# Performance work log

Measured on AMD Instinct MI355X. Metric: run time of the kernel, lower is better.

## Reference

```python
import jax, jax.numpy as jnp
import numpy as np


def _adder2d(x, w, stride, padding):
    """AdderNet 'convolution': out[b,o,i,j] = -sum_p |patch[b,p,i,j] - w[o,p]|.

    x: [B, C, H, W], w: [O, C, kh, kw]. Patches are extracted in (C, kh, kw)
    channel-major order, matching torch.nn.functional.unfold / w.reshape(O, -1).
    """
    O, C, kh, kw = w.shape
    patches = jax.lax.conv_general_dilated_patches(
        x, (kh, kw), (stride, stride), [(padding, padding), (padding, padding)])
    B, P, Ho, Wo = patches.shape  # P = C*kh*kw
    p = patches.reshape(B, P, Ho * Wo)
    wf = w.reshape(O, P)

    def per_out(wo):  # sequential over small O to avoid a [B,O,P,L] blowup
        return -jnp.sum(jnp.abs(p - wo[None, :, None]), axis=1)  # [B, L]

    out = jax.lax.map(per_out, wf)  # [O, B, L]
    return jnp.transpose(out, (1, 0, 2)).reshape(B, O, Ho, Wo)


def setup_inputs() -> dict:
    key = jax.random.key(0)
    ks = jax.random.split(key, 5)
    x = jax.random.normal(ks[0], (4096, 1, 28, 28), dtype=jnp.float32)
    w1 = jax.random.normal(ks[1], (16, 1, 3, 3), dtype=jnp.float32)
    w2 = jax.random.normal(ks[2], (32, 16, 3, 3), dtype=jnp.float32)
    w3 = jax.random.normal(ks[3], (16, 32, 3, 3), dtype=jnp.float32)
    w4 = jax.random.normal(ks[4], (10, 16, 3, 3), dtype=jnp.float32)
    return {"x": x, "w1": w1, "w2": w2, "w3": w3, "w4": w4}


def reference(x, w1, w2, w3, w4):
    h = x - 0.5
    h = jax.nn.relu((_adder2d(h, w1, 2, 0) + 10.0) / 4.0)   # [B,16,13,13]
    h = jax.nn.relu((_adder2d(h, w2, 2, 1) + 130.0) / 8.0)  # [B,32,7,7]
    h = jax.nn.relu((_adder2d(h, w3, 2, 1) + 280.0) / 16.0)  # [B,16,4,4]
    h = _adder2d(h, w4, 2, 0)                                # [B,10,1,1]
    h = h.reshape(h.shape[0], -1)                            # [B,10]
    return jax.nn.log_softmax(h, axis=1)
```

## Files before the change

### kernel.cpp

```cpp
#include <hip/hip_runtime.h>
#include <math.h>


#if defined(__has_builtin)
#if __has_builtin(__builtin_amdgcn_sad_u16)
#define HAS_SAD 1
#endif
#endif

__device__ __forceinline__ unsigned sadu16(unsigned a, unsigned b, unsigned acc) {
#ifdef HAS_SAD
  return __builtin_amdgcn_sad_u16(a, b, acc);
#else
  int al = (int)(a & 0xFFFFu), ah = (int)(a >> 16);
  int bl = (int)(b & 0xFFFFu), bh = (int)(b >> 16);
  return acc + (unsigned)(al > bl ? al - bl : bl - al)
             + (unsigned)(ah > bh ? ah - bh : bh - ah);
#endif
}

__device__ __forceinline__ unsigned quant(float v) {
  return (unsigned)fmaf(v, 1024.0f, 8192.5f);
}

#define QPAD 0x20002000u

__global__ void adder_prep(const float* __restrict__ w1, const float* __restrict__ w2,
                           const float* __restrict__ w3, const float* __restrict__ w4,
                           unsigned* __restrict__ qw) {
  int k = blockIdx.x * 256 + threadIdx.x;
  if (k < 96) {
    int o = k / 6, r = k % 6, kh = r >> 1, h = r & 1;
    const float* p = w1 + o * 9 + kh * 3;
    qw[k] = h ? quant(p[2]) : (quant(p[0]) | (quant(p[1]) << 16));
  } else if (k < 2400) {
    int k2 = k - 96, m = k2 / 288, r = k2 % 288, o = r / 9, pk = r % 9;
    int s = o * 144 + 2 * m * 9 + pk;
    qw[k] = quant(w2[s]) | (quant(w2[s + 9]) << 16);
  } else if (k < 4704) {
    int k3 = k - 2400, m2 = k3 / 144, r = k3 % 144, o = r / 9, pk = r % 9;
    int s = o * 288 + 2 * m2 * 9 + pk;
    qw[k] = quant(w3[s]) | (quant(w3[s + 9]) << 16);
  } else if (k < 5424) {
    int k4 = k - 4704, m = k4 / 90, r = k4 % 90, o = r / 9, pk = r % 9;
    int s = o * 144 + 2 * m * 9 + pk;
    qw[k] = quant(w4[s]) | (quant(w4[s + 9]) << 16);
  }
}

__global__ __launch_bounds__(256, 2) void adder_main(
    const float* __restrict__ gx,
    const unsigned* __restrict__ qw,
    float* __restrict__ gout)
{
  __shared__ __align__(16) unsigned sA1[9600];
  __shared__ __align__(16) unsigned sA2[5760];
  __shared__ __align__(16) unsigned sX[2016];

  const int t = threadIdx.x;
  const int b = blockIdx.x;

  for (int k = t; k < 1568; k += 256) {
    int img = k / 392, r = k % 392, y = r / 14, xw = r % 14;
    const float2 v = *(const float2*)(gx + (size_t)(4 * b + img) * 784 + y * 28 + 2 * xw);
    sX[img * 504 + y * 18 + xw] = quant(v.x - 0.5f) | (quant(v.y - 0.5f) << 16);
  }
  for (int k = t; k < 448; k += 256) {
    int img = k / 112, r = k % 112, y = r / 4, c = r % 4;
    sX[img * 504 + y * 18 + 14 + c] = 0u;
  }
  {
    uint4 pad4 = make_uint4(QPAD, QPAD, QPAD, QPAD);
    uint4* p = (uint4*)sA1;
    for (int k = t; k < 2400; k += 256) p[k] = pad4;
    uint4* p2 = (uint4*)sA2;
    for (int k = t; k < 1440; k += 256) p2[k] = pad4;
  }
  __syncthreads();

  if (t < 208) {
    const int i = t >> 4, img = (t >> 2) & 3, jq = t & 3;
    unsigned r[3][5], mw[3][4];
#pragma unroll
    for (int kh = 0; kh < 3; ++kh) {
      const unsigned* rp = sX + img * 504 + (2 * i + kh) * 18 + 4 * jq;
#pragma unroll
      for (int c = 0; c < 5; ++c) r[kh][c] = rp[c];
#pragma unroll
      for (int c = 0; c < 4; ++c) mw[kh][c] = r[kh][c + 1] & 0xFFFFu;
    }
#pragma unroll 1
    for (int op = 0; op < 8; ++op) {
      const unsigned* w = qw + op * 12;
      unsigned a0[4], a1[4];
#pragma unroll
      for (int jj = 0; jj < 4; ++jj) { a0[jj] = 0u; a1[jj] = 0u; }
#pragma unroll
      for (int kh = 0; kh < 3; ++kh) {
        unsigned wa01 = w[kh * 2], wa2 = w[kh * 2 + 1];
        unsigned wb01 = w[6 + kh * 2], wb2 = w[6 + kh * 2 + 1];
#pragma unroll
        for (int jj = 0; jj < 4; ++jj) {
          a0[jj] = sadu16(r[kh][jj], wa01, a0[jj]);
          a0[jj] = sadu16(mw[kh][jj], wa2, a0[jj]);
          a1[jj] = sadu16(r[kh][jj], wb01, a1[jj]);
          a1[jj] = sadu16(mw[kh][jj], wb2, a1[jj]);
        }
      }
      unsigned* dst = sA1 + (op * 4 + img) * 300 + (i + 1) * 20 + 4 * jq + 1;
#pragma unroll
      for (int jj = 0; jj < 4; ++jj) {
        if (4 * jq + jj < 13) {
          float f0 = fmaxf(fmaf((float)a0[jj], -1.0f / 4096.0f, 2.5f), 0.0f);
          float f1 = fmaxf(fmaf((float)a1[jj], -1.0f / 4096.0f, 2.5f), 0.0f);
          dst[jj] = quant(f0) | (quant(f1) << 16);
        }
      }
    }
  }
  __syncthreads();

  if (t < 196) {
    const int img = t / 49, pos = t % 49, i = pos / 7, j = pos % 7;
    unsigned acc[32];
#pragma unroll
    for (int o = 0; o < 32; ++o) acc[o] = 0u;
    const unsigned* qw2 = qw + 96;
#pragma unroll 1
    for (int m = 0; m < 8; ++m) {
      const unsigned* plane = sA1 + (m * 4 + img) * 300;
      unsigned p[3][3];
#pragma unroll
      for (int kh = 0; kh < 3; ++kh)
#pragma unroll
        for (int c = 0; c < 3; ++c)
          p[kh][c] = plane[(2 * i + kh) * 20 + 2 * j + c];
      const unsigned* wm = qw2 + m * 288;
#pragma unroll
      for (int oct = 0; oct < 4; ++oct) {
        const unsigned* ws = wm + oct * 72;
#pragma unroll
        for (int oo = 0; oo < 8; ++oo) {
          const unsigned* w9 = ws + oo * 9;
          unsigned a = acc[oct * 8 + oo];
#pragma unroll
          for (int kh = 0; kh < 3; ++kh)
#pragma unroll
            for (int c = 0; c < 3; ++c)
              a = sadu16(p[kh][c], w9[kh * 3 + c], a);
          acc[oct * 8 + oo] = a;
        }
      }
    }
#pragma unroll
    for (int m2 = 0; m2 < 16; ++m2) {
      float f0 = fmaxf(fmaf((float)acc[2 * m2],     -1.0f / 8192.0f, 16.25f), 0.0f);
      float f1 = fmaxf(fmaf((float)acc[2 * m2 + 1], -1.0f / 8192.0f, 16.25f), 0.0f);
      sA2[(m2 * 4 + img) * 90 + (i + 1) * 10 + (j + 1)] = quant(f0) | (quant(f1) << 16);
    }
  }
  __syncthreads();

  if (t < 128) {
    const int mg = t >> 6, img = (t >> 4) & 3, pos = t & 15, i = pos >> 2, j = pos & 3;
    unsigned acc[16];
#pragma unroll
    for (int o = 0; o < 16; ++o) acc[o] = 0u;
    const unsigned* qw3 = qw + 2400;
#pragma unroll 1
    for (int mm = 0; mm < 8; ++mm) {
      const int m2 = mg * 8 + mm;
      const unsigned* plane = sA2 + (m2 * 4 + img) * 90;
      unsigned p[3][3];
#pragma unroll
      for (int kh = 0; kh < 3; ++kh)
#pragma unroll
        for (int c = 0; c < 3; ++c)
          p[kh][c] = plane[(2 * i + kh) * 10 + 2 * j + c];
      const unsigned* wm = qw3 + m2 * 144;
#pragma unroll
      for (int oct = 0; oct < 2; ++oct) {
        const unsigned* ws = wm + oct * 72;
#pragma unroll
        for (int oo = 0; oo < 8; ++oo) {
          const unsigned* w9 = ws + oo * 9;
          unsigned a = acc[oct * 8 + oo];
#pragma unroll
          for (int kh = 0; kh < 3; ++kh)
#pragma unroll
            for (int c = 0; c < 3; ++c)
              a = sadu16(p[kh][c], w9[kh * 3 + c], a);
          acc[oct * 8 + oo] = a;
        }
      }
    }
    unsigned* pp = sA1 + ((mg * 4 + img) * 16 + pos) * 20;
#pragma unroll
    for (int u = 0; u < 4; ++u)
      *(uint4*)(pp + u * 4) = make_uint4(acc[4 * u], acc[4 * u + 1], acc[4 * u + 2], acc[4 * u + 3]);
  }
  __syncthreads();

  if (t < 64) {
    const int img = t >> 4, pos = t & 15;
    const unsigned* P = sA1 + (img * 16 + pos) * 20;
    const unsigned* Q = P + 1280;
#pragma unroll
    for (int m = 0; m < 8; ++m) {
      unsigned s0 = P[2 * m] + Q[2 * m];
      unsigned s1 = P[2 * m + 1] + Q[2 * m + 1];
      float f0 = fmaxf(fmaf((float)s0, -1.0f / 16384.0f, 17.5f), 0.0f);
      float f1 = fmaxf(fmaf((float)s1, -1.0f / 16384.0f, 17.5f), 0.0f);
      sA1[2560 + (img * 8 + m) * 18 + pos] = quant(f0) | (quant(f1) << 16);
    }
  }
  __syncthreads();

  if (t < 160) {
    const int img = t / 40, r = t % 40, o = r / 4, mq = r % 4;
    const unsigned* qw4 = qw + 4704;
    unsigned acc = 0u;
#pragma unroll
    for (int mm = 0; mm < 2; ++mm) {
      const int m = mq * 2 + mm;
      const unsigned* a3 = sA1 + 2560 + (img * 8 + m) * 18;
      const unsigned* w9 = qw4 + (m * 10 + o) * 9;
#pragma unroll
      for (int kh = 0; kh < 3; ++kh)
#pragma unroll
        for (int kw = 0; kw < 3; ++kw)
          acc = sadu16(a3[kh * 4 + kw], w9[kh * 3 + kw], acc);
    }
    sA1[3136 + t] = acc;
  }
  __syncthreads();
  if (t < 40) {
    const int img = t / 10, o = t % 10;
    const unsigned* P = sA1 + 3136 + img * 40 + o * 4;
    unsigned s = P[0] + P[1] + P[2] + P[3];
    ((float*)sA1)[3296 + t] = -(float)s * (1.0f / 1024.0f);
  }
  __syncthreads();
  if (t < 40) {
    const int img = t / 10, o = t % 10;
    const float* lg = (const float*)sA1 + 3296 + img * 10;
    float mx = lg[0];
#pragma unroll
    for (int k = 1; k < 10; ++k) mx = fmaxf(mx, lg[k]);
    float sum = 0.0f;
#pragma unroll
    for (int k = 0; k < 10; ++k) sum += __expf(lg[k] - mx);
    gout[(size_t)(4 * b + img) * 10 + o] = lg[o] - mx - __logf(sum);
  }
}

extern "C" void kernel_launch(void* const* d_in, const int* in_sizes, int n_in,
                              void* d_out, int out_size, void* d_ws, size_t ws_size,
                              hipStream_t stream) {
  const float* x  = (const float*)d_in[0];
  const float* w1 = (const float*)d_in[1];
  const float* w2 = (const float*)d_in[2];
  const float* w3 = (const float*)d_in[3];
  const float* w4 = (const float*)d_in[4];
  unsigned* qw = (unsigned*)d_ws;
  float* out = (float*)d_out;
  adder_prep<<<22, 256, 0, stream>>>(w1, w2, w3, w4, qw);
  adder_main<<<1024, 256, 0, stream>>>(x, qw, out);
}
```

Baseline: 125.5 us.

## Shrink shared memory with tighter plane strides and border-only padding for three blocks per CU

Shared memory is cut from about 69KB to about 53KB by merging the input and layer-2 buffers, using odd strides (17, 9) instead of padded ones, and writing QPAD only to plane borders instead of filling whole buffers. Launch bounds are raised to 3 blocks per SM so more blocks can be resident. Layer 3 now uses all 256 threads (8 outputs each instead of 16 on 128 threads), and idle threads in layer 2 fill the next buffer's borders. The risks are tighter register limits under the higher occupancy target and new LDS bank-conflict patterns from the odd strides.

```diff
diff --git a/kernel.cpp b/kernel.cpp
--- a/kernel.cpp
+++ b/kernel.cpp
@@ -48,14 +48,13 @@
   }
 }
 
-__global__ __launch_bounds__(256, 2) void adder_main(
+__global__ __launch_bounds__(256, 3) void adder_main(
     const float* __restrict__ gx,
     const unsigned* __restrict__ qw,
     float* __restrict__ gout)
 {
-  __shared__ __align__(16) unsigned sA1[9600];
-  __shared__ __align__(16) unsigned sA2[5760];
-  __shared__ __align__(16) unsigned sX[2016];
+  __shared__ __align__(16) unsigned sA1[8160];
+  __shared__ __align__(16) unsigned sU[5184];
 
   const int t = threadIdx.x;
   const int b = blockIdx.x;
@@ -63,18 +62,16 @@
   for (int k = t; k < 1568; k += 256) {
     int img = k / 392, r = k % 392, y = r / 14, xw = r % 14;
     const float2 v = *(const float2*)(gx + (size_t)(4 * b + img) * 784 + y * 28 + 2 * xw);
-    sX[img * 504 + y * 18 + xw] = quant(v.x - 0.5f) | (quant(v.y - 0.5f) << 16);
-  }
-  for (int k = t; k < 448; k += 256) {
-    int img = k / 112, r = k % 112, y = r / 4, c = r % 4;
-    sX[img * 504 + y * 18 + 14 + c] = 0u;
-  }
-  {
-    uint4 pad4 = make_uint4(QPAD, QPAD, QPAD, QPAD);
-    uint4* p = (uint4*)sA1;
-    for (int k = t; k < 2400; k += 256) p[k] = pad4;
-    uint4* p2 = (uint4*)sA2;
-    for (int k = t; k < 1440; k += 256) p2[k] = pad4;
+    sU[img * 476 + y * 17 + xw] = quant(v.x - 0.5f) | (quant(v.y - 0.5f) << 16);
+  }
+  for (int k = t; k < 1792; k += 256) {
+    int plane = k / 56, c = k % 56;
+    int y, x;
+    if (c < 15)      { y = 0;      x = c; }
+    else if (c < 30) { y = 14;     x = c - 15; }
+    else if (c < 43) { y = c - 29; x = 0; }
+    else             { y = c - 42; x = 14; }
+    sA1[plane * 255 + y * 17 + x] = QPAD;
   }
   __syncthreads();
 
@@ -83,7 +80,7 @@
     unsigned r[3][5], mw[3][4];
 #pragma unroll
     for (int kh = 0; kh < 3; ++kh) {
-      const unsigned* rp = sX + img * 504 + (2 * i + kh) * 18 + 4 * jq;
+      const unsigned* rp = sU + img * 476 + (2 * i + kh) * 17 + 4 * jq;
 #pragma unroll
       for (int c = 0; c < 5; ++c) r[kh][c] = rp[c];
 #pragma unroll
@@ -107,7 +104,7 @@
           a1[jj] = sadu16(mw[kh][jj], wb2, a1[jj]);
         }
       }
-      unsigned* dst = sA1 + (op * 4 + img) * 300 + (i + 1) * 20 + 4 * jq + 1;
+      unsigned* dst = sA1 + (op * 4 + img) * 255 + (i + 1) * 17 + 4 * jq + 1;
 #pragma unroll
       for (int jj = 0; jj < 4; ++jj) {
         if (4 * jq + jj < 13) {
@@ -128,13 +125,13 @@
     const unsigned* qw2 = qw + 96;
 #pragma unroll 1
     for (int m = 0; m < 8; ++m) {
-      const unsigned* plane = sA1 + (m * 4 + img) * 300;
+      const unsigned* plane = sA1 + (m * 4 + img) * 255;
       unsigned p[3][3];
 #pragma unroll
       for (int kh = 0; kh < 3; ++kh)
 #pragma unroll
         for (int c = 0; c < 3; ++c)
-          p[kh][c] = plane[(2 * i + kh) * 20 + 2 * j + c];
+          p[kh][c] = plane[(2 * i + kh) * 17 + 2 * j + c];
       const unsigned* wm = qw2 + m * 288;
 #pragma unroll
       for (int oct = 0; oct < 4; ++oct) {
@@ -156,62 +153,68 @@
     for (int m2 = 0; m2 < 16; ++m2) {
       float f0 = fmaxf(fmaf((float)acc[2 * m2],     -1.0f / 8192.0f, 16.25f), 0.0f);
       float f1 = fmaxf(fmaf((float)acc[2 * m2 + 1], -1.0f / 8192.0f, 16.25f), 0.0f);
-      sA2[(m2 * 4 + img) * 90 + (i + 1) * 10 + (j + 1)] = quant(f0) | (quant(f1) << 16);
-    }
-  }
-  __syncthreads();
-
-  if (t < 128) {
-    const int mg = t >> 6, img = (t >> 4) & 3, pos = t & 15, i = pos >> 2, j = pos & 3;
-    unsigned acc[16];
-#pragma unroll
-    for (int o = 0; o < 16; ++o) acc[o] = 0u;
+      sU[(m2 * 4 + img) * 81 + (i + 1) * 9 + (j + 1)] = quant(f0) | (quant(f1) << 16);
+    }
+  } else {
+    for (int k = t - 196; k < 2048; k += 60) {
+      int plane = k >> 5, c = k & 31;
+      int y, x;
+      if (c < 9)       { y = 0; x = c; }
+      else if (c < 18) { y = 8; x = c - 9; }
+      else if (c < 25) { y = c - 17; x = 0; }
+      else             { y = c - 24; x = 8; }
+      sU[plane * 81 + y * 9 + x] = QPAD;
+    }
+  }
+  __syncthreads();
+
+  {
+    const int pos = t & 15, img = (t >> 4) & 3, og = (t >> 6) & 1, mg = t >> 7;
+    const int i = pos >> 2, j = pos & 3;
+    unsigned acc[8];
+#pragma unroll
+    for (int o = 0; o < 8; ++o) acc[o] = 0u;
     const unsigned* qw3 = qw + 2400;
 #pragma unroll 1
     for (int mm = 0; mm < 8; ++mm) {
       const int m2 = mg * 8 + mm;
-      const unsigned* plane = sA2 + (m2 * 4 + img) * 90;
+      const unsigned* plane = sU + (m2 * 4 + img) * 81;
       unsigned p[3][3];
 #pragma unroll
       for (int kh = 0; kh < 3; ++kh)
 #pragma unroll
         for (int c = 0; c < 3; ++c)
-          p[kh][c] = plane[(2 * i + kh) * 10 + 2 * j + c];
-      const unsigned* wm = qw3 + m2 * 144;
-#pragma unroll
-      for (int oct = 0; oct < 2; ++oct) {
-        const unsigned* ws = wm + oct * 72;
-#pragma unroll
-        for (int oo = 0; oo < 8; ++oo) {
-          const unsigned* w9 = ws + oo * 9;
-          unsigned a = acc[oct * 8 + oo];
-#pragma unroll
-          for (int kh = 0; kh < 3; ++kh)
-#pragma unroll
-            for (int c = 0; c < 3; ++c)
-              a = sadu16(p[kh][c], w9[kh * 3 + c], a);
-          acc[oct * 8 + oo] = a;
-        }
-      }
-    }
-    unsigned* pp = sA1 + ((mg * 4 + img) * 16 + pos) * 20;
-#pragma unroll
-    for (int u = 0; u < 4; ++u)
-      *(uint4*)(pp + u * 4) = make_uint4(acc[4 * u], acc[4 * u + 1], acc[4 * u + 2], acc[4 * u + 3]);
+          p[kh][c] = plane[(2 * i + kh) * 9 + 2 * j + c];
+      const unsigned* ws = qw3 + m2 * 144 + og * 72;
+#pragma unroll
+      for (int oo = 0; oo < 8; ++oo) {
+        const unsigned* w9 = ws + oo * 9;
+        unsigned a = acc[oo];
+#pragma unroll
+        for (int kh = 0; kh < 3; ++kh)
+#pragma unroll
+          for (int c = 0; c < 3; ++c)
+            a = sadu16(p[kh][c], w9[kh * 3 + c], a);
+        acc[oo] = a;
+      }
+    }
+    unsigned* pp = sA1 + t * 12;
+    *(uint4*)(pp)     = make_uint4(acc[0], acc[1], acc[2], acc[3]);
+    *(uint4*)(pp + 4) = make_uint4(acc[4], acc[5], acc[6], acc[7]);
   }
   __syncthreads();
 
   if (t < 64) {
     const int img = t >> 4, pos = t & 15;
-    const unsigned* P = sA1 + (img * 16 + pos) * 20;
-    const unsigned* Q = P + 1280;
 #pragma unroll
     for (int m = 0; m < 8; ++m) {
-      unsigned s0 = P[2 * m] + Q[2 * m];
-      unsigned s1 = P[2 * m + 1] + Q[2 * m + 1];
+      const int og = m >> 2, oo = 2 * (m & 3);
+      const int b0 = ((og << 6) | (img << 4) | pos) * 12;
+      unsigned s0 = sA1[b0 + oo]     + sA1[b0 + 1536 + oo];
+      unsigned s1 = sA1[b0 + oo + 1] + sA1[b0 + 1536 + oo + 1];
       float f0 = fmaxf(fmaf((float)s0, -1.0f / 16384.0f, 17.5f), 0.0f);
       float f1 = fmaxf(fmaf((float)s1, -1.0f / 16384.0f, 17.5f), 0.0f);
-      sA1[2560 + (img * 8 + m) * 18 + pos] = quant(f0) | (quant(f1) << 16);
+      sA1[3104 + (img * 8 + m) * 17 + pos] = quant(f0) | (quant(f1) << 16);
     }
   }
   __syncthreads();
@@ -223,7 +226,7 @@
 #pragma unroll
     for (int mm = 0; mm < 2; ++mm) {
       const int m = mq * 2 + mm;
-      const unsigned* a3 = sA1 + 2560 + (img * 8 + m) * 18;
+      const unsigned* a3 = sA1 + 3104 + (img * 8 + m) * 17;
       const unsigned* w9 = qw4 + (m * 10 + o) * 9;
 #pragma unroll
       for (int kh = 0; kh < 3; ++kh)
@@ -231,19 +234,19 @@
         for (int kw = 0; kw < 3; ++kw)
           acc = sadu16(a3[kh * 4 + kw], w9[kh * 3 + kw], acc);
     }
-    sA1[3136 + t] = acc;
+    sA1[3712 + t] = acc;
   }
   __syncthreads();
   if (t < 40) {
     const int img = t / 10, o = t % 10;
-    const unsigned* P = sA1 + 3136 + img * 40 + o * 4;
+    const unsigned* P = sA1 + 3712 + img * 40 + o * 4;
     unsigned s = P[0] + P[1] + P[2] + P[3];
-    ((float*)sA1)[3296 + t] = -(float)s * (1.0f / 1024.0f);
+    ((float*)sA1)[3968 + t] = -(float)s * (1.0f / 1024.0f);
   }
   __syncthreads();
   if (t < 40) {
     const int img = t / 10, o = t % 10;
-    const float* lg = (const float*)sA1 + 3296 + img * 10;
+    const float* lg = (const float*)sA1 + 3968 + img * 10;
     float mx = lg[0];
 #pragma unroll
     for (int k = 1; k < 10; ++k) mx = fmaxf(mx, lg[k]);
```

Measured after the change: 119.3 us. -4.9%, faster.
